# Performance work log

Hardware: AMD Instinct MI355X
Metric: run time of the kernel (lower is better)

## Reference

```python
import jax, jax.numpy as jnp
import numpy as np

D = 128
H = 4
L = 3
MAX_LEN = 696


def _pe(max_len, d):
    pos = jnp.arange(max_len, dtype=jnp.float32)[:, None]
    div = jnp.exp(jnp.arange(0, d, 2, dtype=jnp.float32) * (-jnp.log(jnp.float32(10000.0)) / d))
    pe = jnp.zeros((max_len, d), dtype=jnp.float32)
    pe = pe.at[:, 0::2].set(jnp.sin(pos * div))
    pe = pe.at[:, 1::2].set(jnp.cos(pos * div))
    return pe  # [max_len, d]


def _ln(x, w, b, eps=1e-5):
    m = jnp.mean(x, axis=-1, keepdims=True)
    v = jnp.mean((x - m) ** 2, axis=-1, keepdims=True)
    return (x - m) / jnp.sqrt(v + eps) * w + b


def _mha(xq, xkv, wqkv, bqkv, wo, bo, mask=None):
    # xq: [Tq,B,d], xkv: [Tk,B,d] (seq-first, torch convention)
    d = xq.shape[-1]
    hd = d // H
    q = xq @ wqkv[:d].T + bqkv[:d]
    k = xkv @ wqkv[d:2 * d].T + bqkv[d:2 * d]
    v = xkv @ wqkv[2 * d:].T + bqkv[2 * d:]

    def split(t):
        T, B, _ = t.shape
        return t.reshape(T, B, H, hd).transpose(1, 2, 0, 3)  # [B,H,T,hd]

    qh, kh, vh = split(q), split(k), split(v)
    s = jnp.einsum('bhqd,bhkd->bhqk', qh, kh) / jnp.sqrt(jnp.float32(hd))
    if mask is not None:
        s = jnp.where(mask, jnp.float32(-1e9), s)
    a = jax.nn.softmax(s, axis=-1)
    o = jnp.einsum('bhqk,bhkd->bhqd', a, vh)
    Tq, B = xq.shape[0], xq.shape[1]
    o = o.transpose(2, 0, 1, 3).reshape(Tq, B, d)
    return o @ wo.T + bo


def _forward(src, tgt, emb_in_w, emb_in_b, emb_out_w, emb_out_b,
             enc_qkv_w, enc_qkv_b, enc_proj_w, enc_proj_b,
             enc_ff1_w, enc_ff1_b, enc_ff2_w, enc_ff2_b, enc_ln_w, enc_ln_b,
             dec_sa_qkv_w, dec_sa_qkv_b, dec_sa_proj_w, dec_sa_proj_b,
             dec_ca_qkv_w, dec_ca_qkv_b, dec_ca_proj_w, dec_ca_proj_b,
             dec_ff1_w, dec_ff1_b, dec_ff2_w, dec_ff2_b, dec_ln_w, dec_ln_b,
             head_w, head_b):
    pe = _pe(MAX_LEN, D)
    # ---- encoder ----
    src_p = jnp.transpose(src, (2, 0, 1))  # [S,B,1]
    x = src_p @ emb_in_w.T + emb_in_b + pe[:src_p.shape[0], None, :]
    for i in range(L):
        a = _mha(x, x, enc_qkv_w[i], enc_qkv_b[i], enc_proj_w[i], enc_proj_b[i])
        x = _ln(x + a, enc_ln_w[i, 0], enc_ln_b[i, 0])
        f = jax.nn.relu(x @ enc_ff1_w[i].T + enc_ff1_b[i]) @ enc_ff2_w[i].T + enc_ff2_b[i]
        x = _ln(x + f, enc_ln_w[i, 1], enc_ln_b[i, 1])
    memory = x  # [S,B,D]
    # ---- decoder (full teacher forcing: loop collapses to one causal pass) ----
    tgt_p = jnp.transpose(tgt, (2, 0, 1))  # [T,B,1]
    T = tgt_p.shape[0]
    y = tgt_p[:T - 1] @ emb_out_w.T + emb_out_b  # [T-1,B,D]
    # original code applies pos encoding only to the initial token of the decode loop
    y = y.at[0].add(pe[0])
    mask = jnp.triu(jnp.ones((T - 1, T - 1), dtype=bool), k=1)  # True = masked
    for i in range(L):
        a = _mha(y, y, dec_sa_qkv_w[i], dec_sa_qkv_b[i], dec_sa_proj_w[i], dec_sa_proj_b[i], mask=mask)
        y = _ln(y + a, dec_ln_w[i, 0], dec_ln_b[i, 0])
        c = _mha(y, memory, dec_ca_qkv_w[i], dec_ca_qkv_b[i], dec_ca_proj_w[i], dec_ca_proj_b[i])
        y = _ln(y + c, dec_ln_w[i, 1], dec_ln_b[i, 1])
        f = jax.nn.relu(y @ dec_ff1_w[i].T + dec_ff1_b[i]) @ dec_ff2_w[i].T + dec_ff2_b[i]
        y = _ln(y + f, dec_ln_w[i, 2], dec_ln_b[i, 2])
    out = y @ head_w.T + head_b  # [T-1,B,1]
    return jnp.transpose(out, (1, 2, 0))  # [B,1,T-1]


def setup_inputs() -> dict:
    key = jax.random.key(0)
    ks = iter(jax.random.split(key, 64))

    def n(shape, s=0.02):
        return (jax.random.normal(next(ks), shape) * s).astype(jnp.float32)

    return {
        'src': jax.random.normal(next(ks), (64, 1, 696), dtype=jnp.float32),
        'tgt': jax.random.normal(next(ks), (64, 1, 512), dtype=jnp.float32),
        'emb_in_w': n((D, 1)), 'emb_in_b': n((D,)),
        'emb_out_w': n((D, 1)), 'emb_out_b': n((D,)),
        'enc_qkv_w': n((L, 3 * D, D)), 'enc_qkv_b': n((L, 3 * D)),
        'enc_proj_w': n((L, D, D)), 'enc_proj_b': n((L, D)),
        'enc_ff1_w': n((L, D, D)), 'enc_ff1_b': n((L, D)),
        'enc_ff2_w': n((L, D, D)), 'enc_ff2_b': n((L, D)),
        'enc_ln_w': jnp.ones((L, 2, D), dtype=jnp.float32),
        'enc_ln_b': jnp.zeros((L, 2, D), dtype=jnp.float32),
        'dec_sa_qkv_w': n((L, 3 * D, D)), 'dec_sa_qkv_b': n((L, 3 * D)),
        'dec_sa_proj_w': n((L, D, D)), 'dec_sa_proj_b': n((L, D)),
        'dec_ca_qkv_w': n((L, 3 * D, D)), 'dec_ca_qkv_b': n((L, 3 * D)),
        'dec_ca_proj_w': n((L, D, D)), 'dec_ca_proj_b': n((L, D)),
        'dec_ff1_w': n((L, D, D)), 'dec_ff1_b': n((L, D)),
        'dec_ff2_w': n((L, D, D)), 'dec_ff2_b': n((L, D)),
        'dec_ln_w': jnp.ones((L, 3, D), dtype=jnp.float32),
        'dec_ln_b': jnp.zeros((L, 3, D), dtype=jnp.float32),
        'head_w': n((1, D)), 'head_b': n((1,)),
    }


def reference(src, tgt, emb_in_w, emb_in_b, emb_out_w, emb_out_b,
              enc_qkv_w, enc_qkv_b, enc_proj_w, enc_proj_b,
              enc_ff1_w, enc_ff1_b, enc_ff2_w, enc_ff2_b, enc_ln_w, enc_ln_b,
              dec_sa_qkv_w, dec_sa_qkv_b, dec_sa_proj_w, dec_sa_proj_b,
              dec_ca_qkv_w, dec_ca_qkv_b, dec_ca_proj_w, dec_ca_proj_b,
              dec_ff1_w, dec_ff1_b, dec_ff2_w, dec_ff2_b, dec_ln_w, dec_ln_b,
              head_w, head_b):
    return _forward(src, tgt, emb_in_w, emb_in_b, emb_out_w, emb_out_b,
                    enc_qkv_w, enc_qkv_b, enc_proj_w, enc_proj_b,
                    enc_ff1_w, enc_ff1_b, enc_ff2_w, enc_ff2_b, enc_ln_w, enc_ln_b,
                    dec_sa_qkv_w, dec_sa_qkv_b, dec_sa_proj_w, dec_sa_proj_b,
                    dec_ca_qkv_w, dec_ca_qkv_b, dec_ca_proj_w, dec_ca_proj_b,
                    dec_ff1_w, dec_ff1_b, dec_ff2_w, dec_ff2_b, dec_ln_w, dec_ln_b,
                    head_w, head_b)
```

## Files before the change

### kernel.cpp

```cpp
#include <hip/hip_runtime.h>
#include <hip/hip_bf16.h>


typedef unsigned short u16;
typedef unsigned int u32;
typedef float f32x4 __attribute__((ext_vector_type(4)));
typedef float f32x2 __attribute__((ext_vector_type(2)));
typedef float f32x16 __attribute__((ext_vector_type(16)));
typedef unsigned short u16x8 __attribute__((ext_vector_type(8)));
typedef unsigned int u32x2 __attribute__((ext_vector_type(2)));
typedef unsigned int u32x4 __attribute__((ext_vector_type(4)));
typedef __bf16 bf16x8 __attribute__((ext_vector_type(8)));

static __device__ __forceinline__ float bf2f(u16 u) {
  u32 x = ((u32)u) << 16;
  return __builtin_bit_cast(float, x);
}
static __device__ __forceinline__ u16 f2bf(float f) {
  u32 x = __builtin_bit_cast(u32, f);
  u32 r = (x + 0x7fffu + ((x >> 16) & 1u)) >> 16;
  return (u16)r;
}
static __device__ __forceinline__ f32x4 mfma16(bf16x8 a, bf16x8 b, f32x4 c) {
  return __builtin_amdgcn_mfma_f32_16x16x32_bf16(a, b, c, 0, 0, 0);
}
static __device__ __forceinline__ f32x16 mfma32(bf16x8 a, bf16x8 b, f32x16 c) {
  return __builtin_amdgcn_mfma_f32_32x32x16_bf16(a, b, c, 0, 0, 0);
}
static __device__ __forceinline__ void plswap(u32& a, u32& b) {
  u32x2 r = __builtin_amdgcn_permlane32_swap(a, b, false, false);
  a = r.x; b = r.y;
}

__global__ void detect_k(const u32* __restrict__ ones, int* __restrict__ flag) {
  *flag = (ones[0] == 0x3F803F80u) ? 1 : 0;
}

struct CvtArgs {
  const void* p[32];
  int n[32];
  int off[32];
};

__global__ __launch_bounds__(256) void cvt_all(CvtArgs A, const int* __restrict__ flag,
                                               float* __restrict__ poolf,
                                               u16* __restrict__ poolb) {
  int ti = blockIdx.y;
  int i = blockIdx.x * 256 + threadIdx.x;
  int n = A.n[ti];
  if (i >= n) return;
  int o = A.off[ti] + i;
  if (*flag) {
    u16 raw = ((const u16*)A.p[ti])[i];
    poolb[o] = raw;
    poolf[o] = bf2f(raw);
  } else {
    float v = ((const float*)A.p[ti])[i];
    poolf[o] = v;
    poolb[o] = f2bf(v);
  }
}

__global__ void embed_enc(const float* __restrict__ src, const float* __restrict__ w,
                          const float* __restrict__ b, float* __restrict__ X,
                          u16* __restrict__ Xb) {
  int s = blockIdx.x, d = threadIdx.x;
  float freq = __expf(-(float)(d & 126) * 0.07195578415606394f);
  float arg = (float)s * freq;
  float pe = (d & 1) ? cosf(arg) : sinf(arg);
  float wd = w[d], bd = b[d];
  for (int bb = 0; bb < 64; ++bb) {
    float v = src[bb * 696 + s] * wd + bd + pe;
    size_t o = ((size_t)s * 64 + bb) * 128 + d;
    X[o] = v;
    Xb[o] = f2bf(v);
  }
}

__global__ void embed_dec(const float* __restrict__ tgt, const float* __restrict__ w,
                          const float* __restrict__ b, float* __restrict__ Y,
                          u16* __restrict__ Yb) {
  int tt = blockIdx.x, d = threadIdx.x;
  float wd = w[d], bd = b[d];
  float pe0 = (tt == 0 && (d & 1)) ? 1.0f : 0.0f;
  for (int bb = 0; bb < 64; ++bb) {
    float v = tgt[bb * 512 + tt] * wd + bd + pe0;
    size_t o = ((size_t)tt * 64 + bb) * 128 + d;
    Y[o] = v;
    Yb[o] = f2bf(v);
  }
}

__global__ __launch_bounds__(256) void gemm_ff(
    const u16* __restrict__ Xb, const u16* __restrict__ W1,
    const float* __restrict__ b1, const u16* __restrict__ W2,
    const float* __restrict__ b2, float* __restrict__ R,
    u16* __restrict__ Rb, const float* __restrict__ lnw,
    const float* __restrict__ lnb) {
  __shared__ u16 Ws[128][136];
  __shared__ u16 Hs[64][136];
  const int t = threadIdx.x;
  const int n0 = blockIdx.x << 6;
  const int wv = t >> 6, lane = t & 63, lg = lane >> 4, lr = lane & 15;
  const int r0 = n0 + (wv << 4);

#pragma unroll
  for (int i = 0; i < 8; ++i) {
    int idx = t + (i << 8);
    int r = idx >> 4, c = (idx & 15) << 3;
    *(u16x8*)&Ws[r][c] = *(const u16x8*)(W1 + ((size_t)r << 7) + c);
  }
  bf16x8 afr[4];
  const int arow = r0 + lr;
#pragma unroll
  for (int ks = 0; ks < 4; ++ks)
    afr[ks] = *(const bf16x8*)(Xb + ((size_t)arow << 7) + (ks << 5) + (lg << 3));
  __syncthreads();

  f32x4 acc[8] = {};
#pragma unroll
  for (int ks = 0; ks < 4; ++ks) {
#pragma unroll
    for (int cb = 0; cb < 8; ++cb) {
      bf16x8 bfr = *(const bf16x8*)&Ws[(cb << 4) + lr][(ks << 5) + (lg << 3)];
      acc[cb] = mfma16(afr[ks], bfr, acc[cb]);
    }
  }
#pragma unroll
  for (int cb = 0; cb < 8; ++cb) {
    float bv = b1[(cb << 4) + lr];
#pragma unroll
    for (int r = 0; r < 4; ++r) {
      float v = fmaxf(acc[cb][r] + bv, 0.0f);
      Hs[(wv << 4) + (lg << 2) + r][(cb << 4) + lr] = f2bf(v);
    }
  }
  __syncthreads();

#pragma unroll
  for (int i = 0; i < 8; ++i) {
    int idx = t + (i << 8);
    int r = idx >> 4, c = (idx & 15) << 3;
    *(u16x8*)&Ws[r][c] = *(const u16x8*)(W2 + ((size_t)r << 7) + c);
  }
  __syncthreads();

  bf16x8 hfr[4];
#pragma unroll
  for (int ks = 0; ks < 4; ++ks)
    hfr[ks] = *(const bf16x8*)&Hs[(wv << 4) + lr][(ks << 5) + (lg << 3)];
#pragma unroll
  for (int cb = 0; cb < 8; ++cb) acc[cb] = f32x4{0, 0, 0, 0};
#pragma unroll
  for (int ks = 0; ks < 4; ++ks) {
#pragma unroll
    for (int cb = 0; cb < 8; ++cb) {
      bf16x8 bfr = *(const bf16x8*)&Ws[(cb << 4) + lr][(ks << 5) + (lg << 3)];
      acc[cb] = mfma16(hfr[ks], bfr, acc[cb]);
    }
  }

  float vals[8][4];
#pragma unroll
  for (int cb = 0; cb < 8; ++cb) {
    float bv = b2[(cb << 4) + lr];
#pragma unroll
    for (int r = 0; r < 4; ++r) {
      size_t row = (size_t)(r0 + (lg << 2) + r);
      vals[cb][r] = acc[cb][r] + bv + R[(row << 7) + (cb << 4) + lr];
    }
  }
  float mean[4], rstd[4];
#pragma unroll
  for (int r = 0; r < 4; ++r) {
    float s = 0.0f, s2 = 0.0f;
#pragma unroll
    for (int cb = 0; cb < 8; ++cb) {
      float v = vals[cb][r];
      s += v; s2 += v * v;
    }
    s += __shfl_xor(s, 1); s2 += __shfl_xor(s2, 1);
    s += __shfl_xor(s, 2); s2 += __shfl_xor(s2, 2);
    s += __shfl_xor(s, 4); s2 += __shfl_xor(s2, 4);
    s += __shfl_xor(s, 8); s2 += __shfl_xor(s2, 8);
    float m = s * 0.0078125f;
    float var = s2 * 0.0078125f - m * m;
    mean[r] = m;
    rstd[r] = rsqrtf(var + 1e-5f);
  }
#pragma unroll
  for (int cb = 0; cb < 8; ++cb) {
    float w = lnw[(cb << 4) + lr], bb = lnb[(cb << 4) + lr];
#pragma unroll
    for (int r = 0; r < 4; ++r) {
      float v = (vals[cb][r] - mean[r]) * rstd[r] * w + bb;
      size_t o = ((size_t)(r0 + (lg << 2) + r) << 7) + (cb << 4) + lr;
      R[o] = v;
      Rb[o] = f2bf(v);
    }
  }
}

__global__ __launch_bounds__(256) void gemm_qkv(
    const u16* __restrict__ Xb, const u16* __restrict__ Wb,
    const float* __restrict__ bias, u16* __restrict__ Qg,
    u16* __restrict__ Kg, u16* __restrict__ Vg, int M, int kbase, int vbase) {
  __shared__ u16 Xs[64][136];
  __shared__ u16 Ws[64][136];
  const int t = threadIdx.x;
  const int n0 = blockIdx.x << 6, m0 = blockIdx.y << 6;
  const int wq = t >> 6, lane = t & 63, lg = lane >> 4, lr = lane & 15;
  const int wr = (wq >> 1) << 5, wc = (wq & 1) << 5;
  const float QS = 0.17677669529663687f * 1.4426950408889634f;

#pragma unroll
  for (int i = 0; i < 4; ++i) {
    int idx = t + (i << 8);
    int r = idx >> 4, c = (idx & 15) << 3;
    *(u16x8*)&Xs[r][c] = *(const u16x8*)(Xb + (size_t)(n0 + r) * 128 + c);
    *(u16x8*)&Ws[r][c] = *(const u16x8*)(Wb + (size_t)(m0 + r) * 128 + c);
  }
  __syncthreads();

  f32x4 acc00 = {0,0,0,0}, acc01 = {0,0,0,0}, acc10 = {0,0,0,0}, acc11 = {0,0,0,0};
#pragma unroll
  for (int ks = 0; ks < 4; ++ks) {
    bf16x8 a0 = *(const bf16x8*)&Xs[wr + lr][(ks << 5) + (lg << 3)];
    bf16x8 a1 = *(const bf16x8*)&Xs[wr + 16 + lr][(ks << 5) + (lg << 3)];
    bf16x8 b0 = *(const bf16x8*)&Ws[wc + lr][(ks << 5) + (lg << 3)];
    bf16x8 b1 = *(const bf16x8*)&Ws[wc + 16 + lr][(ks << 5) + (lg << 3)];
    acc00 = mfma16(a0, b0, acc00);
    acc01 = mfma16(a0, b1, acc01);
    acc10 = mfma16(a1, b0, acc10);
    acc11 = mfma16(a1, b1, acc11);
  }

  f32x4 accs[2][2] = {{acc00, acc01}, {acc10, acc11}};
#pragma unroll
  for (int mi = 0; mi < 2; ++mi) {
#pragma unroll
    for (int ni = 0; ni < 2; ++ni) {
      int col = m0 + wc + (ni << 4) + lr;
      float bv = bias[col];
#pragma unroll
      for (int r = 0; r < 4; ++r) {
        int row = n0 + wr + (mi << 4) + (lg << 2) + r;
        float v = accs[mi][ni][r] + bv;
        size_t ro = (size_t)row << 7;
        if (col < kbase) {
          Qg[ro + col] = f2bf(v * QS);
        } else if (col < vbase) {
          Kg[ro + (col - kbase)] = f2bf(v);
        } else {
          Vg[ro + (col - vbase)] = f2bf(v);
        }
      }
    }
  }
}

__global__ __launch_bounds__(256) void attn_pl(
    const u16* __restrict__ Qg, const u16* __restrict__ Kg,
    const u16* __restrict__ Vg, const u16* __restrict__ Wp,
    const float* __restrict__ bp, float* __restrict__ R,
    u16* __restrict__ Rb, const float* __restrict__ lnw,
    const float* __restrict__ lnb, int Tq, int Tk, int causal, int nstrips) {
  __shared__ u16 KOs[64][132];
  __shared__ __align__(16) u16 VW[128][74];
  __shared__ float Lw[4][2][36];
  u16* VWf = &VW[0][0];
  const int t = threadIdx.x;
  const int wv = t >> 6, lane = t & 63;
  const int lq = lane & 31, hi = lane >> 5;
  const int lr16 = lane & 15, lg16 = lane >> 4;
  const int h = wv;
  const int p = blockIdx.x;
  const int idx = p >> 3;
  const int b = ((p & 7) << 3) + idx / nstrips;
  const int strip = idx % nstrips;
  const int q0 = strip << 6;

  bf16x8 qf[2][2];
#pragma unroll
  for (int ss = 0; ss < 2; ++ss) {
    int ql = q0 + (ss << 5) + lq; if (ql > Tq - 1) ql = Tq - 1;
    const u16* qp = Qg + (((size_t)ql * 64 + b) << 7) + h * 32 + (hi << 3);
    qf[ss][0] = *(const bf16x8*)qp;
    qf[ss][1] = *(const bf16x8*)(qp + 16);
  }

  f32x16 o[2] = {};
  float lsum[2] = {0.0f, 0.0f};

  const int ntb = causal ? (strip + 1) : (((Tk - 1) >> 6) + 1);

  const int vtok = t >> 2, vj = (t & 3) << 3;

  for (int kt = 0; kt < ntb; ++kt) {
    const int k0 = kt << 6;
    __syncthreads();
#pragma unroll
    for (int i = 0; i < 4; ++i) {
      int sidx = t + (i << 8);
      int row = sidx >> 4, c8 = (sidx & 15) << 3;
      int tok = k0 + row; if (tok > Tk - 1) tok = Tk - 1;
      *(u16x8*)&KOs[row][c8] = *(const u16x8*)(Kg + (((size_t)tok * 64 + b) << 7) + c8);
    }
    {
      int tokv = k0 + vtok; if (tokv > Tk - 1) tokv = Tk - 1;
      const u16* vb = Vg + (((size_t)tokv * 64 + b) << 7);
#pragma unroll
      for (int pass = 0; pass < 4; ++pass) {
        int d0 = (pass << 5) + vj;
        u16x8 vvv = *(const u16x8*)(vb + d0);
#pragma unroll
        for (int e = 0; e < 8; ++e) VW[d0 + e][vtok] = vvv[e];
      }
    }
    __syncthreads();

#pragma unroll
    for (int ss = 0; ss < 2; ++ss) {
      const int qs = q0 + (ss << 5);
      if (qs >= Tq) continue;
      int lastc = causal ? qs + 31 : Tk - 1;
      if (lastc > Tk - 1) lastc = Tk - 1;
      if (kt > (lastc >> 6)) continue;
      const int nfull = causal ? (qs >> 6) : (Tk >> 6);
      const bool masked = (kt >= nfull);

#pragma unroll
      for (int kb = 0; kb < 2; ++kb) {
        const int krow = (kb << 5) + lq;
        bf16x8 ka0 = *(const bf16x8*)&KOs[krow][h * 32 + (hi << 3)];
        bf16x8 ka1 = *(const bf16x8*)&KOs[krow][h * 32 + 16 + (hi << 3)];
        f32x16 s = {};
        __builtin_amdgcn_s_setprio(1);
        s = mfma32(ka0, qf[ss][0], s);
        s = mfma32(ka1, qf[ss][1], s);
        __builtin_amdgcn_s_setprio(0);

        float pvv[16];
#pragma unroll
        for (int r = 0; r < 16; ++r) {
          float sv = s[r];
          if (masked) {
            int kk = k0 + (kb << 5) + (r & 3) + ((r >> 2) << 3) + (hi << 2);
            int q = qs + lq;
            bool ok = causal ? (kk <= q) : (kk < Tk);
            sv = ok ? sv : -1e30f;
          }
          float e = exp2f(sv);
          pvv[r] = e;
          lsum[ss] += e;
        }
        u32 u[8];
#pragma unroll
        for (int m = 0; m < 8; ++m)
          asm("v_cvt_pk_bf16_f32 %0, %1, %2" : "=v"(u[m]) : "v"(pvv[2 * m]), "v"(pvv[2 * m + 1]));

#pragma unroll
        for (int c = 0; c < 2; ++c) {
          u32 a0 = u[4 * c + 0], b0 = u[4 * c + 2];
          u32 a1 = u[4 * c + 1], b1 = u[4 * c + 3];
          plswap(a0, b0);
          plswap(a1, b1);
          u32x4 wv4 = {a0, a1, b0, b1};
          bf16x8 pf = __builtin_bit_cast(bf16x8, wv4);
          bf16x8 vf = *(const bf16x8*)&VW[h * 32 + lq][(kb << 5) + (c << 4) + (hi << 3)];
          __builtin_amdgcn_s_setprio(1);
          o[ss] = mfma32(pf, vf, o[ss]);
          __builtin_amdgcn_s_setprio(0);
        }
      }
    }
  }

#pragma unroll
  for (int ss = 0; ss < 2; ++ss) {
    float lt = lsum[ss] + __shfl_xor(lsum[ss], 32);
    if (hi == 0) Lw[wv][ss][lq] = lt > 0.0f ? 1.0f / lt : 0.0f;
  }
  __syncthreads();

#pragma unroll
  for (int ss = 0; ss < 2; ++ss) {
    f32x4 li[4];
#pragma unroll
    for (int g = 0; g < 4; ++g)
      li[g] = *(const f32x4*)&Lw[wv][ss][(hi << 2) + (g << 3)];
#pragma unroll
    for (int r = 0; r < 16; ++r) {
      int qrow = (ss << 5) + (r & 3) + ((r >> 2) << 3) + (hi << 2);
      KOs[qrow][h * 32 + lq] = f2bf(o[ss][r] * li[r >> 2][r & 3]);
    }
  }

  float vals[2][4][4];
#pragma unroll
  for (int ch = 0; ch < 2; ++ch) {
    __syncthreads();
#pragma unroll
    for (int i = 0; i < 4; ++i) {
      int sidx = t + (i << 8);
      int row = sidx >> 4, c8 = (sidx & 15) << 3;
      *(u16x8*)&VWf[row * 132 + c8] = *(const u16x8*)(Wp + ((size_t)((ch << 6) + row) << 7) + c8);
    }
    __syncthreads();

    f32x4 acc[4] = {};
#pragma unroll
    for (int ks = 0; ks < 4; ++ks) {
      bf16x8 af = *(const bf16x8*)&KOs[(wv << 4) + lr16][(ks << 5) + (lg16 << 3)];
#pragma unroll
      for (int cb = 0; cb < 4; ++cb) {
        bf16x8 bf = *(const bf16x8*)&VWf[((cb << 4) + lr16) * 132 + (ks << 5) + (lg16 << 3)];
        acc[cb] = mfma16(af, bf, acc[cb]);
      }
    }
#pragma unroll
    for (int cb = 0; cb < 4; ++cb) {
      int col = (ch << 6) + (cb << 4) + lr16;
      float bv = bp[col];
#pragma unroll
      for (int r = 0; r < 4; ++r) {
        int q = q0 + (wv << 4) + (lg16 << 2) + r;
        int qc = q > Tq - 1 ? Tq - 1 : q;
        vals[ch][cb][r] = acc[cb][r] + bv + R[(((size_t)qc * 64 + b) << 7) + col];
      }
    }
  }

#pragma unroll
  for (int r = 0; r < 4; ++r) {
    float s = 0.0f, s2 = 0.0f;
#pragma unroll
    for (int ch = 0; ch < 2; ++ch)
#pragma unroll
      for (int cb = 0; cb < 4; ++cb) {
        float v = vals[ch][cb][r];
        s += v; s2 += v * v;
      }
    s += __shfl_xor(s, 1); s2 += __shfl_xor(s2, 1);
    s += __shfl_xor(s, 2); s2 += __shfl_xor(s2, 2);
    s += __shfl_xor(s, 4); s2 += __shfl_xor(s2, 4);
    s += __shfl_xor(s, 8); s2 += __shfl_xor(s2, 8);
    float m = s * 0.0078125f;
    float rstd = rsqrtf(s2 * 0.0078125f - m * m + 1e-5f);
    int q = q0 + (wv << 4) + (lg16 << 2) + r;
    if (q < Tq) {
      size_t base = (((size_t)q * 64 + b) << 7);
#pragma unroll
      for (int ch = 0; ch < 2; ++ch)
#pragma unroll
        for (int cb = 0; cb < 4; ++cb) {
          int col = (ch << 6) + (cb << 4) + lr16;
          float v = (vals[ch][cb][r] - m) * rstd * lnw[col] + lnb[col];
          R[base + col] = v;
          Rb[base + col] = f2bf(v);
        }
    }
  }
}

__global__ __launch_bounds__(256) void head_k(
    const float* __restrict__ Y, const float* __restrict__ w,
    const float* __restrict__ bh, void* __restrict__ out, const int* __restrict__ flag) {
  int n = (blockIdx.x << 2) + (threadIdx.x >> 6);
  int lane = threadIdx.x & 63;
  const float* yp = Y + (size_t)n * 128 + (lane << 1);
  float s = yp[0] * w[lane << 1] + yp[1] * w[(lane << 1) + 1];
#pragma unroll
  for (int off = 1; off < 64; off <<= 1) s += __shfl_xor(s, off);
  if (lane == 0) {
    int tt = n >> 6, bb = n & 63;
    float r = s + bh[0];
    int idx = bb * 511 + tt;
    if (*flag) ((u16*)out)[idx] = f2bf(r);
    else       ((float*)out)[idx] = r;
  }
}

extern "C" void kernel_launch(void* const* d_in, const int* in_sizes, int n_in,
                              void* d_out, int out_size, void* d_ws, size_t ws_size,
                              hipStream_t stream) {
  (void)out_size; (void)ws_size;
  CvtArgs A;
  long off[33]; off[0] = 0;
  int maxn = 0;
  for (int i = 0; i < 32; ++i) {
    int n = (i < n_in) ? in_sizes[i] : 0;
    A.p[i] = (i < n_in) ? d_in[i] : d_in[0];
    A.n[i] = n;
    A.off[i] = (int)off[i];
    off[i + 1] = off[i] + n;
    if (n > maxn) maxn = n;
  }
  const size_t offA = (size_t)((off[32] + 15) & ~15l);

  const size_t NE = 44544;
  const size_t ND = 32704;
  float* ws   = (float*)d_ws;
  int*   flag = (int*)d_ws;
  float* Wp   = ws + 16;
  float* Xe   = Wp + offA;
  float* Yd   = Xe + NE * 128;
  u16*   U    = (u16*)(Yd + ND * 128);
  u16*   Wb   = U;
  u16*   Xebf = Wb + offA;
  u16*   Ydbf = Xebf + NE * 128;
  u16*   Qgb  = Ydbf + ND * 128;
  u16*   Kgb  = Qgb + NE * 128;
  u16*   Vgb  = Kgb + NE * 128;

  const float* F = Wp;
  detect_k<<<1, 1, 0, stream>>>((const u32*)d_in[14], flag);
  cvt_all<<<dim3((maxn + 255) / 256, 32), 256, 0, stream>>>(A, flag, Wp, Wb);

  embed_enc<<<dim3(696), dim3(128), 0, stream>>>(F + A.off[0], F + A.off[2], F + A.off[3], Xe, Xebf);
  for (int i = 0; i < 3; ++i) {
    gemm_qkv<<<dim3(696, 6), 256, 0, stream>>>(Xebf, Wb + A.off[6] + i * 49152, F + A.off[7] + i * 384,
                                               Qgb, Kgb, Vgb, 384, 128, 256);
    attn_pl<<<dim3(704), 256, 0, stream>>>(Qgb, Kgb, Vgb,
                                           Wb + A.off[8] + i * 16384, F + A.off[9] + i * 128,
                                           Xe, Xebf,
                                           F + A.off[14] + (i * 2 + 0) * 128, F + A.off[15] + (i * 2 + 0) * 128,
                                           696, 696, 0, 11);
    gemm_ff<<<dim3(696), 256, 0, stream>>>(Xebf, Wb + A.off[10] + i * 16384, F + A.off[11] + i * 128,
                                           Wb + A.off[12] + i * 16384, F + A.off[13] + i * 128,
                                           Xe, Xebf, F + A.off[14] + (i * 2 + 1) * 128, F + A.off[15] + (i * 2 + 1) * 128);
  }

  embed_dec<<<dim3(511), dim3(128), 0, stream>>>(F + A.off[1], F + A.off[4], F + A.off[5], Yd, Ydbf);
  for (int i = 0; i < 3; ++i) {
    gemm_qkv<<<dim3(511, 6), 256, 0, stream>>>(Ydbf, Wb + A.off[16] + i * 49152, F + A.off[17] + i * 384,
                                               Qgb, Kgb, Vgb, 384, 128, 256);
    attn_pl<<<dim3(512), 256, 0, stream>>>(Qgb, Kgb, Vgb,
                                           Wb + A.off[18] + i * 16384, F + A.off[19] + i * 128,
                                           Yd, Ydbf,
                                           F + A.off[28] + (i * 3 + 0) * 128, F + A.off[29] + (i * 3 + 0) * 128,
                                           511, 511, 1, 8);
    gemm_qkv<<<dim3(511, 2), 256, 0, stream>>>(Ydbf, Wb + A.off[20] + i * 49152, F + A.off[21] + i * 384,
                                               Qgb, nullptr, nullptr, 128, 128, 128);
    gemm_qkv<<<dim3(696, 4), 256, 0, stream>>>(Xebf, Wb + A.off[20] + i * 49152 + 16384, F + A.off[21] + i * 384 + 128,
                                               nullptr, Kgb, Vgb, 256, 0, 128);
    attn_pl<<<dim3(512), 256, 0, stream>>>(Qgb, Kgb, Vgb,
                                           Wb + A.off[22] + i * 16384, F + A.off[23] + i * 128,
                                           Yd, Ydbf,
                                           F + A.off[28] + (i * 3 + 1) * 128, F + A.off[29] + (i * 3 + 1) * 128,
                                           511, 696, 0, 8);
    gemm_ff<<<dim3(511), 256, 0, stream>>>(Ydbf, Wb + A.off[24] + i * 16384, F + A.off[25] + i * 128,
                                           Wb + A.off[26] + i * 16384, F + A.off[27] + i * 128,
                                           Yd, Ydbf, F + A.off[28] + (i * 3 + 2) * 128, F + A.off[29] + (i * 3 + 2) * 128);
  }

  head_k<<<dim3(8176), 256, 0, stream>>>(Yd, F + A.off[30], F + A.off[31], d_out, flag);
}
```

Measured before the change: 889.8 us.

## Process 128 query rows per attention block with 8 waves sharing K/V tiles

The fused attention+projection kernel now runs 512 threads per block, with two groups of four head-waves each handling 64 query rows. This doubles the query strip to 128 rows, so each staged K/V tile in shared memory serves twice as many queries, halving global K/V reloads and the grid size. Shared memory is reorganised into a pool aliasing K, transposed V and the output tile, plus a separate projection-weight buffer. The trade-off is fewer blocks, which lowers parallelism on the 64-batch grids, and extra causal work from wasted tiles in the larger strips.

```diff
diff --git a/kernel.cpp b/kernel.cpp
--- a/kernel.cpp
+++ b/kernel.cpp
@@ -259,31 +259,34 @@
   }
 }
 
-__global__ __launch_bounds__(256) void attn_pl(
+__global__ __launch_bounds__(512) void attn_pl(
     const u16* __restrict__ Qg, const u16* __restrict__ Kg,
     const u16* __restrict__ Vg, const u16* __restrict__ Wp,
     const float* __restrict__ bp, float* __restrict__ R,
     u16* __restrict__ Rb, const float* __restrict__ lnw,
     const float* __restrict__ lnb, int Tq, int Tk, int causal, int nstrips) {
-  __shared__ u16 KOs[64][132];
-  __shared__ __align__(16) u16 VW[128][74];
-  __shared__ float Lw[4][2][36];
-  u16* VWf = &VW[0][0];
+  __shared__ u16 POOL[17920];
+  __shared__ u16 Wsh[64][132];
+  __shared__ float Lw[8][2][36];
+  u16 (*Ks)[132] = (u16(*)[132])POOL;
+  u16 (*VW)[74]  = (u16(*)[74])(POOL + 8448);
+  u16* Of = POOL;
   const int t = threadIdx.x;
   const int wv = t >> 6, lane = t & 63;
   const int lq = lane & 31, hi = lane >> 5;
   const int lr16 = lane & 15, lg16 = lane >> 4;
-  const int h = wv;
+  const int h = wv & 3, qh = wv >> 2;
   const int p = blockIdx.x;
   const int idx = p >> 3;
   const int b = ((p & 7) << 3) + idx / nstrips;
   const int strip = idx % nstrips;
-  const int q0 = strip << 6;
+  const int q0 = strip << 7;
+  const int qbase = q0 + (qh << 6);
 
   bf16x8 qf[2][2];
 #pragma unroll
   for (int ss = 0; ss < 2; ++ss) {
-    int ql = q0 + (ss << 5) + lq; if (ql > Tq - 1) ql = Tq - 1;
+    int ql = qbase + (ss << 5) + lq; if (ql > Tq - 1) ql = Tq - 1;
     const u16* qp = Qg + (((size_t)ql * 64 + b) << 7) + h * 32 + (hi << 3);
     qf[ss][0] = *(const bf16x8*)qp;
     qf[ss][1] = *(const bf16x8*)(qp + 16);
@@ -292,26 +295,28 @@
   f32x16 o[2] = {};
   float lsum[2] = {0.0f, 0.0f};
 
-  const int ntb = causal ? (strip + 1) : (((Tk - 1) >> 6) + 1);
-
-  const int vtok = t >> 2, vj = (t & 3) << 3;
+  const int maxtb = ((Tk - 1) >> 6) + 1;
+  int ntb = causal ? (((q0 + 127) >> 6) + 1) : maxtb;
+  if (ntb > maxtb) ntb = maxtb;
+
+  const int vtok = t >> 3, vj = (t & 7) << 3;
 
   for (int kt = 0; kt < ntb; ++kt) {
     const int k0 = kt << 6;
     __syncthreads();
 #pragma unroll
-    for (int i = 0; i < 4; ++i) {
-      int sidx = t + (i << 8);
+    for (int i = 0; i < 2; ++i) {
+      int sidx = t + (i << 9);
       int row = sidx >> 4, c8 = (sidx & 15) << 3;
       int tok = k0 + row; if (tok > Tk - 1) tok = Tk - 1;
-      *(u16x8*)&KOs[row][c8] = *(const u16x8*)(Kg + (((size_t)tok * 64 + b) << 7) + c8);
+      *(u16x8*)&Ks[row][c8] = *(const u16x8*)(Kg + (((size_t)tok * 64 + b) << 7) + c8);
     }
     {
       int tokv = k0 + vtok; if (tokv > Tk - 1) tokv = Tk - 1;
       const u16* vb = Vg + (((size_t)tokv * 64 + b) << 7);
 #pragma unroll
-      for (int pass = 0; pass < 4; ++pass) {
-        int d0 = (pass << 5) + vj;
+      for (int pass = 0; pass < 2; ++pass) {
+        int d0 = (pass << 6) + vj;
         u16x8 vvv = *(const u16x8*)(vb + d0);
 #pragma unroll
         for (int e = 0; e < 8; ++e) VW[d0 + e][vtok] = vvv[e];
@@ -321,7 +326,7 @@
 
 #pragma unroll
     for (int ss = 0; ss < 2; ++ss) {
-      const int qs = q0 + (ss << 5);
+      const int qs = qbase + (ss << 5);
       if (qs >= Tq) continue;
       int lastc = causal ? qs + 31 : Tk - 1;
       if (lastc > Tk - 1) lastc = Tk - 1;
@@ -332,8 +337,8 @@
 #pragma unroll
       for (int kb = 0; kb < 2; ++kb) {
         const int krow = (kb << 5) + lq;
-        bf16x8 ka0 = *(const bf16x8*)&KOs[krow][h * 32 + (hi << 3)];
-        bf16x8 ka1 = *(const bf16x8*)&KOs[krow][h * 32 + 16 + (hi << 3)];
+        bf16x8 ka0 = *(const bf16x8*)&Ks[krow][h * 32 + (hi << 3)];
+        bf16x8 ka1 = *(const bf16x8*)&Ks[krow][h * 32 + 16 + (hi << 3)];
         f32x16 s = {};
         __builtin_amdgcn_s_setprio(1);
         s = mfma32(ka0, qf[ss][0], s);
@@ -391,8 +396,8 @@
       li[g] = *(const f32x4*)&Lw[wv][ss][(hi << 2) + (g << 3)];
 #pragma unroll
     for (int r = 0; r < 16; ++r) {
-      int qrow = (ss << 5) + (r & 3) + ((r >> 2) << 3) + (hi << 2);
-      KOs[qrow][h * 32 + lq] = f2bf(o[ss][r] * li[r >> 2][r & 3]);
+      int qrow = (qh << 6) + (ss << 5) + (r & 3) + ((r >> 2) << 3) + (hi << 2);
+      Of[qrow * 132 + h * 32 + lq] = f2bf(o[ss][r] * li[r >> 2][r & 3]);
     }
   }
 
@@ -401,20 +406,20 @@
   for (int ch = 0; ch < 2; ++ch) {
     __syncthreads();
 #pragma unroll
-    for (int i = 0; i < 4; ++i) {
-      int sidx = t + (i << 8);
+    for (int i = 0; i < 2; ++i) {
+      int sidx = t + (i << 9);
       int row = sidx >> 4, c8 = (sidx & 15) << 3;
-      *(u16x8*)&VWf[row * 132 + c8] = *(const u16x8*)(Wp + ((size_t)((ch << 6) + row) << 7) + c8);
+      *(u16x8*)&Wsh[row][c8] = *(const u16x8*)(Wp + ((size_t)((ch << 6) + row) << 7) + c8);
     }
     __syncthreads();
 
     f32x4 acc[4] = {};
 #pragma unroll
     for (int ks = 0; ks < 4; ++ks) {
-      bf16x8 af = *(const bf16x8*)&KOs[(wv << 4) + lr16][(ks << 5) + (lg16 << 3)];
+      bf16x8 af = *(const bf16x8*)&Of[((wv << 4) + lr16) * 132 + (ks << 5) + (lg16 << 3)];
 #pragma unroll
       for (int cb = 0; cb < 4; ++cb) {
-        bf16x8 bf = *(const bf16x8*)&VWf[((cb << 4) + lr16) * 132 + (ks << 5) + (lg16 << 3)];
+        bf16x8 bf = *(const bf16x8*)&Wsh[(cb << 4) + lr16][(ks << 5) + (lg16 << 3)];
         acc[cb] = mfma16(af, bf, acc[cb]);
       }
     }
@@ -521,11 +526,11 @@
   for (int i = 0; i < 3; ++i) {
     gemm_qkv<<<dim3(696, 6), 256, 0, stream>>>(Xebf, Wb + A.off[6] + i * 49152, F + A.off[7] + i * 384,
                                                Qgb, Kgb, Vgb, 384, 128, 256);
-    attn_pl<<<dim3(704), 256, 0, stream>>>(Qgb, Kgb, Vgb,
+    attn_pl<<<dim3(384), 512, 0, stream>>>(Qgb, Kgb, Vgb,
                                            Wb + A.off[8] + i * 16384, F + A.off[9] + i * 128,
                                            Xe, Xebf,
                                            F + A.off[14] + (i * 2 + 0) * 128, F + A.off[15] + (i * 2 + 0) * 128,
-                                           696, 696, 0, 11);
+                                           696, 696, 0, 6);
     gemm_ff<<<dim3(696), 256, 0, stream>>>(Xebf, Wb + A.off[10] + i * 16384, F + A.off[11] + i * 128,
                                            Wb + A.off[12] + i * 16384, F + A.off[13] + i * 128,
                                            Xe, Xebf, F + A.off[14] + (i * 2 + 1) * 128, F + A.off[15] + (i * 2 + 1) * 128);
@@ -535,20 +540,20 @@
   for (int i = 0; i < 3; ++i) {
     gemm_qkv<<<dim3(511, 6), 256, 0, stream>>>(Ydbf, Wb + A.off[16] + i * 49152, F + A.off[17] + i * 384,
                                                Qgb, Kgb, Vgb, 384, 128, 256);
-    attn_pl<<<dim3(512), 256, 0, stream>>>(Qgb, Kgb, Vgb,
+    attn_pl<<<dim3(256), 512, 0, stream>>>(Qgb, Kgb, Vgb,
                                            Wb + A.off[18] + i * 16384, F + A.off[19] + i * 128,
                                            Yd, Ydbf,
                                            F + A.off[28] + (i * 3 + 0) * 128, F + A.off[29] + (i * 3 + 0) * 128,
-                                           511, 511, 1, 8);
+                                           511, 511, 1, 4);
     gemm_qkv<<<dim3(511, 2), 256, 0, stream>>>(Ydbf, Wb + A.off[20] + i * 49152, F + A.off[21] + i * 384,
                                                Qgb, nullptr, nullptr, 128, 128, 128);
     gemm_qkv<<<dim3(696, 4), 256, 0, stream>>>(Xebf, Wb + A.off[20] + i * 49152 + 16384, F + A.off[21] + i * 384 + 128,
                                                nullptr, Kgb, Vgb, 256, 0, 128);
-    attn_pl<<<dim3(512), 256, 0, stream>>>(Qgb, Kgb, Vgb,
+    attn_pl<<<dim3(256), 512, 0, stream>>>(Qgb, Kgb, Vgb,
                                            Wb + A.off[22] + i * 16384, F + A.off[23] + i * 128,
                                            Yd, Ydbf,
                                            F + A.off[28] + (i * 3 + 1) * 128, F + A.off[29] + (i * 3 + 1) * 128,
-                                           511, 696, 0, 8);
+                                           511, 696, 0, 4);
     gemm_ff<<<dim3(511), 256, 0, stream>>>(Ydbf, Wb + A.off[24] + i * 16384, F + A.off[25] + i * 128,
                                            Wb + A.off[26] + i * 16384, F + A.off[27] + i * 128,
                                            Yd, Ydbf, F + A.off[28] + (i * 3 + 2) * 128, F + A.off[29] + (i * 3 + 2) * 128);
```

New measurement: 939.6 us. 1.06x slower.
